# Kernel optimization log

Hardware: AMD Instinct MI355X
Metric: run time of the kernel (lower is better)

## Reference

```python
import jax, jax.numpy as jnp
import numpy as np

N_NODES = 100000
N_EDGES = 1200000
N_GRAPHS = 2048
VOCAB = 10000
D = 64
C = 2


def setup_inputs() -> dict:
    key = jax.random.key(0)
    ks = jax.random.split(key, 12)
    x = jax.random.randint(ks[0], (N_NODES,), 0, VOCAB)
    edge_index = jax.random.randint(ks[1], (2, N_EDGES), 0, N_NODES)
    batch = jnp.sort(jax.random.randint(ks[2], (N_NODES,), 0, N_GRAPHS))
    s = 0.1
    return {
        'x': x,
        'edge_index': edge_index,
        'batch': batch,
        'emb': jax.random.normal(ks[3], (VOCAB, D), jnp.float32) * s,
        'W1l': jax.random.normal(ks[4], (D, D), jnp.float32) * s,
        'b1l': jnp.zeros((D,), jnp.float32),
        'W1r': jax.random.normal(ks[5], (D, D), jnp.float32) * s,
        'W2l': jax.random.normal(ks[6], (D, D), jnp.float32) * s,
        'b2l': jnp.zeros((D,), jnp.float32),
        'W2r': jax.random.normal(ks[7], (D, D), jnp.float32) * s,
        'Wout': jax.random.normal(ks[8], (C, D), jnp.float32) * s,
        'bout': jnp.zeros((C,), jnp.float32),
    }


def _sage(h, src, dst, Wl, bl, Wr, n_nodes):
    # mean aggregation of source messages onto target nodes (PyG SAGEConv, aggr='mean')
    agg = jax.ops.segment_sum(h[src], dst, num_segments=n_nodes)  # [N, D]
    cnt = jax.ops.segment_sum(jnp.ones((src.shape[0],), h.dtype), dst, num_segments=n_nodes)
    agg = agg / jnp.maximum(cnt, 1.0)[:, None]
    # lin_l(agg) + lin_r(root); lin_l carries the bias, lin_r has none
    return agg @ Wl.T + bl + h @ Wr.T


def reference(x, edge_index, batch, emb, W1l, b1l, W1r, W2l, b2l, W2r, Wout, bout):
    src, dst = edge_index[0], edge_index[1]
    h = emb[x]                                   # [N, D] embedding lookup
    h = jax.nn.relu(_sage(h, src, dst, W1l, b1l, W1r, N_NODES))
    h = jax.nn.relu(_sage(h, src, dst, W2l, b2l, W2r, N_NODES))
    # global mean pool per graph
    pooled = jax.ops.segment_sum(h, batch, num_segments=N_GRAPHS)
    gcnt = jax.ops.segment_sum(jnp.ones((N_NODES,), h.dtype), batch, num_segments=N_GRAPHS)
    pooled = pooled / jnp.maximum(gcnt, 1.0)[:, None]
    return pooled @ Wout.T + bout                # [G, C]
```

## Files before the change

### kernel.cpp

```cpp
#include <hip/hip_runtime.h>

#define NN 100000
#define NE 1200000
#define NG 2048
#define VOCAB 10000
#define D 64
#define C 2

#define NBK 196
#define BSH 9
#define SLOT 7168

typedef _Float16 half8 __attribute__((ext_vector_type(8)));
typedef _Float16 half2 __attribute__((ext_vector_type(2)));

#if __has_builtin(__builtin_amdgcn_fdot2)
#define FDOT2(a, b, c) __builtin_amdgcn_fdot2((a), (b), (c), false)
#else
#define FDOT2(a, b, c) ((float)(a)[0] * (float)(b)[0] + (float)(a)[1] * (float)(b)[1] + (c))
#endif

__device__ __forceinline__ int atomAddI(int* p, int v) {
    return __hip_atomic_fetch_add(p, v, __ATOMIC_RELAXED, __HIP_MEMORY_SCOPE_AGENT);
}
__device__ __forceinline__ void atomAddF(float* p, float v) {
    __hip_atomic_fetch_add(p, v, __ATOMIC_RELAXED, __HIP_MEMORY_SCOPE_AGENT);
}

__global__ void __launch_bounds__(256) k_prepb(const float4* __restrict__ emb4,
        half8* __restrict__ embh,
        const float* __restrict__ W1l, const float* __restrict__ W1r,
        const float* __restrict__ W2l, const float* __restrict__ W2r,
        half2* __restrict__ wp,
        const int* __restrict__ batch, int* __restrict__ gs,
        const int* __restrict__ src, const int* __restrict__ dst,
        int* __restrict__ bcur, unsigned* __restrict__ barr) {
    int blk = blockIdx.x;
    int tid = threadIdx.x;
    if (blk < 313) {
        int i = blk * 256 + tid;
        if (i >= VOCAB * 8) return;
        float4 a = emb4[(size_t)i * 2], b = emb4[(size_t)i * 2 + 1];
        half8 h;
        h[0] = (_Float16)a.x; h[1] = (_Float16)a.y; h[2] = (_Float16)a.z; h[3] = (_Float16)a.w;
        h[4] = (_Float16)b.x; h[5] = (_Float16)b.y; h[6] = (_Float16)b.z; h[7] = (_Float16)b.w;
        embh[i] = h;
    } else if (blk < 345) {
        int i = (blk - 313) * 256 + tid;
        if (i >= 4 * 2048) return;
        int mat = i >> 11, idx = i & 2047;
        const float* W = (mat == 0) ? W1l : (mat == 1) ? W1r : (mat == 2) ? W2l : W2r;
        int row = idx >> 5, kk = idx & 31;
        half2 o;
        o[0] = (_Float16)W[row * 64 + 2 * kk];
        o[1] = (_Float16)W[row * 64 + 2 * kk + 1];
        wp[i] = o;
    } else if (blk < 736) {
        int n = (blk - 345) * 256 + tid;
        if (n >= NN) return;
        int b = batch[n];
        if (n == 0) {
            for (int g = 0; g <= b; ++g) gs[g] = 0;
        } else {
            int bp = batch[n - 1];
            for (int g = bp + 1; g <= b; ++g) gs[g] = n;
        }
        if (n == NN - 1) {
            for (int g = b + 1; g <= NG; ++g) gs[g] = NN;
        }
    } else {
        __shared__ int hcnt[NBK], hbase[NBK], hrank[NBK];
        if (tid < NBK) { hcnt[tid] = 0; hrank[tid] = 0; }
        __syncthreads();
        int bb = blk - 736;
        int per = NE / 384;
        int e0 = bb * per, e1 = e0 + per;
        for (int e = e0 + tid; e < e1; e += 256)
            atomicAdd(&hcnt[dst[e] >> BSH], 1);
        __syncthreads();
        if (tid < NBK) {
            int c = hcnt[tid];
            hbase[tid] = c ? atomAddI(&bcur[tid], c) : 0;
        }
        __syncthreads();
        for (int e = e0 + tid; e < e1; e += 256) {
            int d = dst[e], s = src[e];
            int b = d >> BSH;
            int r = atomicAdd(&hrank[b], 1);
            barr[(size_t)b * SLOT + hbase[b] + r] = ((unsigned)s << BSH) | (unsigned)(d & 511);
        }
    }
}

__global__ void __launch_bounds__(512) k_sortb(const int* __restrict__ bcur,
        const unsigned* __restrict__ barr, const int* __restrict__ x,
        int* __restrict__ start, int* __restrict__ csr, unsigned short* __restrict__ xcsr) {
    __shared__ int cnt[512], loc[512], sm[512];
    int t = threadIdx.x;
    int b = blockIdx.x;
    sm[t] = (t < b && t < NBK) ? bcur[t] : 0;
    cnt[t] = 0;
    __syncthreads();
    for (int off = 1; off < 512; off <<= 1) {
        int v = (t >= off) ? sm[t - off] : 0;
        __syncthreads();
        sm[t] += v;
        __syncthreads();
    }
    int base = sm[511];
    int count = bcur[b];
    const unsigned* bp = barr + (size_t)b * SLOT;
    for (int i = t; i < count; i += 512)
        atomicAdd(&cnt[bp[i] & 511], 1);
    __syncthreads();
    int own = cnt[t];
    sm[t] = own;
    __syncthreads();
    for (int off = 1; off < 512; off <<= 1) {
        int v = (t >= off) ? sm[t - off] : 0;
        __syncthreads();
        sm[t] += v;
        __syncthreads();
    }
    int ex = sm[t] - own;
    loc[t] = ex;
    int g0 = b << BSH;
    if (g0 + t < NN) start[g0 + t] = base + ex;
    if (b == NBK - 1 && t == 0) start[NN] = NE;
    __syncthreads();
    for (int i = t; i < count; i += 512) {
        unsigned p = bp[i];
        int r = atomicAdd(&loc[p & 511], 1);
        int sn = (int)(p >> BSH);
        csr[base + r]  = sn;
        xcsr[base + r] = (unsigned short)x[sn];
    }
}

template<typename IDX>
__device__ __forceinline__ half8 gather_sum(const IDX* __restrict__ idx,
        const half8* __restrict__ g, int f, int s0, int s1) {
    half8 acc = {};
    if (s1 <= s0) return acc;
    const half8 z = {};
    int last = s1 - 1;
    for (int i = s0; i < s1; i += 8) {
        int i1 = min(i + 1, last), i2 = min(i + 2, last), i3 = min(i + 3, last);
        int i4 = min(i + 4, last), i5 = min(i + 5, last), i6 = min(i + 6, last);
        int i7 = min(i + 7, last);
        half8 v0 = g[(size_t)idx[i]  * 8 + f];
        half8 v1 = g[(size_t)idx[i1] * 8 + f];
        half8 v2 = g[(size_t)idx[i2] * 8 + f];
        half8 v3 = g[(size_t)idx[i3] * 8 + f];
        half8 v4 = g[(size_t)idx[i4] * 8 + f];
        half8 v5 = g[(size_t)idx[i5] * 8 + f];
        half8 v6 = g[(size_t)idx[i6] * 8 + f];
        half8 v7 = g[(size_t)idx[i7] * 8 + f];
        v1 = (i + 1 < s1) ? v1 : z;
        v2 = (i + 2 < s1) ? v2 : z;
        v3 = (i + 3 < s1) ? v3 : z;
        v4 = (i + 4 < s1) ? v4 : z;
        v5 = (i + 5 < s1) ? v5 : z;
        v6 = (i + 6 < s1) ? v6 : z;
        v7 = (i + 7 < s1) ? v7 : z;
        acc += ((v0 + v1) + (v2 + v3)) + ((v4 + v5) + (v6 + v7));
    }
    return acc;
}

__global__ void __launch_bounds__(256) k_l1(const int* __restrict__ start,
        const unsigned short* __restrict__ idx, const half8* __restrict__ embh,
        const int* __restrict__ x,
        const half2* __restrict__ wl, const float* __restrict__ bl,
        const half2* __restrict__ wr, half8* __restrict__ h1) {
    __shared__ half8 smA[64][8];
    int tid = threadIdx.x;
    int lane = tid & 63, wave = tid >> 6;

    float pf = 0.f;
    {
        int i = blockIdx.x * 256 + tid;
        if (i < VOCAB * 8) { float4 v = ((const float4*)embh)[i]; pf = v.x * 0.f; }
    }
    asm volatile("" : "+v"(pf));

    int f = lane & 7;
#pragma unroll
    for (int r = 0; r < 2; ++r) {
        int nl = r * 32 + wave * 8 + (lane >> 3);
        int n = blockIdx.x * 64 + nl;
        if (n < NN) {
            int s0 = start[n], s1 = start[n + 1];
            float inv = 1.0f / (float)max(s1 - s0, 1) + pf;
            half8 acc = gather_sum(idx, embh, f, s0, s1);
            half8 o;
#pragma unroll
            for (int k = 0; k < 8; ++k) o[k] = (_Float16)((float)acc[k] * inv);
            smA[nl][f ^ (nl & 7)] = o;
        }
    }
    __syncthreads();

    int h = __builtin_amdgcn_readfirstlane(wave);
    int nn = blockIdx.x * 64 + lane;
    bool valid = nn < NN;
    int n = valid ? nn : NN - 1;

    float acc[16];
#pragma unroll
    for (int d = 0; d < 16; ++d) acc[d] = bl[h * 16 + d];
    const half8* rp = embh + (size_t)x[n] * 8;
    const half2* wlH = wl + (size_t)h * 16 * 32;
    const half2* wrH = wr + (size_t)h * 16 * 32;

    half8 ah = smA[lane][0 ^ (lane & 7)];
    half8 rh = rp[0];
    for (int c = 0; c < 8; ++c) {
        half2 a2[4] = { __builtin_shufflevector(ah, ah, 0, 1),
                        __builtin_shufflevector(ah, ah, 2, 3),
                        __builtin_shufflevector(ah, ah, 4, 5),
                        __builtin_shufflevector(ah, ah, 6, 7) };
        half2 r2[4] = { __builtin_shufflevector(rh, rh, 0, 1),
                        __builtin_shufflevector(rh, rh, 2, 3),
                        __builtin_shufflevector(rh, rh, 4, 5),
                        __builtin_shufflevector(rh, rh, 6, 7) };
        if (c < 7) {
            ah = smA[lane][(c + 1) ^ (lane & 7)];
            rh = rp[c + 1];
        }
        const half2* wlc = wlH + c * 4;
        const half2* wrc = wrH + c * 4;
#pragma unroll
        for (int d = 0; d < 16; ++d) {
#pragma unroll
            for (int kk = 0; kk < 4; ++kk) {
                acc[d] = FDOT2(a2[kk], wlc[d * 32 + kk], acc[d]);
                acc[d] = FDOT2(r2[kk], wrc[d * 32 + kk], acc[d]);
            }
        }
    }

    if (valid) {
        half8 o0, o1;
#pragma unroll
        for (int k = 0; k < 8; ++k) {
            o0[k] = (_Float16)fmaxf(acc[k], 0.f);
            o1[k] = (_Float16)fmaxf(acc[8 + k], 0.f);
        }
        h1[(size_t)n * 8 + 2 * h]     = o0;
        h1[(size_t)n * 8 + 2 * h + 1] = o1;
    }
}

__global__ void __launch_bounds__(256) k_l2(const int* __restrict__ start,
        const int* __restrict__ idx, const half8* __restrict__ h1,
        const int* __restrict__ batch,
        const half2* __restrict__ wl, const float* __restrict__ bl,
        const half2* __restrict__ wr, float* __restrict__ pooled) {
    __shared__ half8 smA[64][8];
    int tid = threadIdx.x;
    int lane = tid & 63, wave = tid >> 6;

    int f = lane & 7;
#pragma unroll
    for (int r = 0; r < 2; ++r) {
        int nl = r * 32 + wave * 8 + (lane >> 3);
        int n = blockIdx.x * 64 + nl;
        if (n < NN) {
            int s0 = start[n], s1 = start[n + 1];
            float inv = 1.0f / (float)max(s1 - s0, 1);
            half8 acc = gather_sum(idx, h1, f, s0, s1);
            half8 o;
#pragma unroll
            for (int k = 0; k < 8; ++k) o[k] = (_Float16)((float)acc[k] * inv);
            smA[nl][f ^ (nl & 7)] = o;
        }
    }
    __syncthreads();

    int h = __builtin_amdgcn_readfirstlane(wave);
    int nn = blockIdx.x * 64 + lane;
    bool valid = nn < NN;
    int n = valid ? nn : NN - 1;

    float acc[16];
#pragma unroll
    for (int d = 0; d < 16; ++d) acc[d] = bl[h * 16 + d];
    const half8* rp = h1 + (size_t)n * 8;
    const half2* wlH = wl + (size_t)h * 16 * 32;
    const half2* wrH = wr + (size_t)h * 16 * 32;

    half8 ah = smA[lane][0 ^ (lane & 7)];
    half8 rh = rp[0];
    for (int c = 0; c < 8; ++c) {
        half2 a2[4] = { __builtin_shufflevector(ah, ah, 0, 1),
                        __builtin_shufflevector(ah, ah, 2, 3),
                        __builtin_shufflevector(ah, ah, 4, 5),
                        __builtin_shufflevector(ah, ah, 6, 7) };
        half2 r2[4] = { __builtin_shufflevector(rh, rh, 0, 1),
                        __builtin_shufflevector(rh, rh, 2, 3),
                        __builtin_shufflevector(rh, rh, 4, 5),
                        __builtin_shufflevector(rh, rh, 6, 7) };
        if (c < 7) {
            ah = smA[lane][(c + 1) ^ (lane & 7)];
            rh = rp[c + 1];
        }
        const half2* wlc = wlH + c * 4;
        const half2* wrc = wrH + c * 4;
#pragma unroll
        for (int d = 0; d < 16; ++d) {
#pragma unroll
            for (int kk = 0; kk < 4; ++kk) {
                acc[d] = FDOT2(a2[kk], wlc[d * 32 + kk], acc[d]);
                acc[d] = FDOT2(r2[kk], wrc[d * 32 + kk], acc[d]);
            }
        }
    }

    int g = batch[n];
    int g1  = __shfl_up(g, 1);
    int g2  = __shfl_up(g, 2);
    int g4  = __shfl_up(g, 4);
    int g8  = __shfl_up(g, 8);
    int g16 = __shfl_up(g, 16);
    int g32 = __shfl_up(g, 32);
    bool s1  = (lane >= 1)  && (g1 == g);
    bool s2  = (lane >= 2)  && (g2 == g);
    bool s4  = (lane >= 4)  && (g4 == g);
    bool s8  = (lane >= 8)  && (g8 == g);
    bool s16 = (lane >= 16) && (g16 == g);
    bool s32 = (lane >= 32) && (g32 == g);
    int gn = __shfl_down(g, 1);
    bool isLast = (lane == 63) || (gn != g);
    float* pg = pooled + (size_t)g * D + h * 16;
#pragma unroll
    for (int d = 0; d < 16; ++d) {
        float v = valid ? fmaxf(acc[d], 0.f) : 0.f;
        float t;
        t = __shfl_up(v, 1);  v += s1  ? t : 0.f;
        t = __shfl_up(v, 2);  v += s2  ? t : 0.f;
        t = __shfl_up(v, 4);  v += s4  ? t : 0.f;
        t = __shfl_up(v, 8);  v += s8  ? t : 0.f;
        t = __shfl_up(v, 16); v += s16 ? t : 0.f;
        t = __shfl_up(v, 32); v += s32 ? t : 0.f;
        if (isLast) atomAddF(pg + d, v);
    }
}

__global__ void __launch_bounds__(256) k_out(const int* __restrict__ gs,
        const float* __restrict__ pooled, const float* __restrict__ Wout,
        const float* __restrict__ bout, float* __restrict__ out) {
    int lane = threadIdx.x & 63;
    int wave = threadIdx.x >> 6;
    int g = blockIdx.x * 4 + wave;
    int s0 = gs[g], s1 = gs[g + 1];
    float p = pooled[(size_t)g * D + lane] / (float)max(s1 - s0, 1);
    float c0 = p * Wout[lane];
    float c1 = p * Wout[D + lane];
#pragma unroll
    for (int off = 32; off > 0; off >>= 1) {
        c0 += __shfl_down(c0, off, 64);
        c1 += __shfl_down(c1, off, 64);
    }
    if (lane == 0) {
        out[g * C + 0] = c0 + bout[0];
        out[g * C + 1] = c1 + bout[1];
    }
}

extern "C" void kernel_launch(void* const* d_in, const int* in_sizes, int n_in,
                              void* d_out, int out_size, void* d_ws, size_t ws_size,
                              hipStream_t stream) {
    const int*   x     = (const int*)d_in[0];
    const int*   src   = (const int*)d_in[1];
    const int*   dst   = src + NE;
    const int*   batch = (const int*)d_in[2];
    const float* emb   = (const float*)d_in[3];
    const float* W1l   = (const float*)d_in[4];
    const float* b1l   = (const float*)d_in[5];
    const float* W1r   = (const float*)d_in[6];
    const float* W2l   = (const float*)d_in[7];
    const float* b2l   = (const float*)d_in[8];
    const float* W2r   = (const float*)d_in[9];
    const float* Wout  = (const float*)d_in[10];
    const float* bout  = (const float*)d_in[11];
    float* out = (float*)d_out;

    _Float16* T0h  = (_Float16*)d_ws;
    _Float16* embh = T0h + (size_t)NN * 64;
    _Float16* wpck = embh + (size_t)VOCAB * 64;
    float* pooled  = (float*)(wpck + 16384);
    int* bcur   = (int*)(pooled + (size_t)NG * 64);
    int* startA = bcur + NBK;
    int* gs     = startA + NN + 1;
    int* csr    = gs + NG + 1;
    unsigned short* xcsr = (unsigned short*)(csr + NE);
    unsigned* barr = (unsigned*)(xcsr + NE);
    half2* wp = (half2*)wpck;

    hipMemsetAsync(pooled, 0, ((size_t)NG * 64 + NBK) * sizeof(float), stream);

    k_prepb<<<1120, 256, 0, stream>>>((const float4*)emb, (half8*)embh,
                                      W1l, W1r, W2l, W2r, wp, batch, gs,
                                      src, dst, bcur, barr);
    k_sortb<<<NBK, 512, 0, stream>>>(bcur, barr, x, startA, csr, xcsr);

    int fusedGrid = (NN + 63) / 64;
    k_l1<<<fusedGrid, 256, 0, stream>>>(startA, xcsr, (const half8*)embh, x,
                                        wp, b1l, wp + 2048, (half8*)T0h);
    k_l2<<<fusedGrid, 256, 0, stream>>>(startA, csr, (const half8*)T0h, batch,
                                        wp + 4096, b2l, wp + 6144, pooled);

    k_out<<<NG / 4, 256, 0, stream>>>(gs, pooled, Wout, bout, out);
}
```

Before: 202.4 us.

## Replace bucketed two-pass CSR sort with per-node count, scan, and atomic placement

CSR construction no longer bins edges into per-bucket staging slots and then locally sorts each bucket in shared memory. It now counts per-node in-degree with global atomics, derives start offsets with a per-bucket scan, and places each edge with a global atomic cursor in a new kernel. This removes the intermediate staging array and the shared-memory sort pass, at the cost of 1.2M global atomics twice, one extra launch, and a nondeterministic edge order within each node's neighbour list.

```diff
diff --git a/kernel.cpp b/kernel.cpp
--- a/kernel.cpp
+++ b/kernel.cpp
@@ -9,7 +9,6 @@
 
 #define NBK 196
 #define BSH 9
-#define SLOT 7168
 
 typedef _Float16 half8 __attribute__((ext_vector_type(8)));
 typedef _Float16 half2 __attribute__((ext_vector_type(2)));
@@ -33,8 +32,8 @@
         const float* __restrict__ W2l, const float* __restrict__ W2r,
         half2* __restrict__ wp,
         const int* __restrict__ batch, int* __restrict__ gs,
-        const int* __restrict__ src, const int* __restrict__ dst,
-        int* __restrict__ bcur, unsigned* __restrict__ barr) {
+        const int* __restrict__ dst,
+        int* __restrict__ bcur, int* __restrict__ ncnt) {
     int blk = blockIdx.x;
     int tid = threadIdx.x;
     if (blk < 313) {
@@ -69,37 +68,31 @@
             for (int g = b + 1; g <= NG; ++g) gs[g] = NN;
         }
     } else {
-        __shared__ int hcnt[NBK], hbase[NBK], hrank[NBK];
-        if (tid < NBK) { hcnt[tid] = 0; hrank[tid] = 0; }
+        __shared__ int hcnt[NBK];
+        if (tid < NBK) hcnt[tid] = 0;
         __syncthreads();
         int bb = blk - 736;
         int per = NE / 384;
         int e0 = bb * per, e1 = e0 + per;
-        for (int e = e0 + tid; e < e1; e += 256)
-            atomicAdd(&hcnt[dst[e] >> BSH], 1);
+        for (int e = e0 + tid; e < e1; e += 256) {
+            int d = dst[e];
+            atomicAdd(&hcnt[d >> BSH], 1);
+            atomAddI(&ncnt[d], 1);
+        }
         __syncthreads();
         if (tid < NBK) {
             int c = hcnt[tid];
-            hbase[tid] = c ? atomAddI(&bcur[tid], c) : 0;
-        }
-        __syncthreads();
-        for (int e = e0 + tid; e < e1; e += 256) {
-            int d = dst[e], s = src[e];
-            int b = d >> BSH;
-            int r = atomicAdd(&hrank[b], 1);
-            barr[(size_t)b * SLOT + hbase[b] + r] = ((unsigned)s << BSH) | (unsigned)(d & 511);
-        }
-    }
-}
-
-__global__ void __launch_bounds__(512) k_sortb(const int* __restrict__ bcur,
-        const unsigned* __restrict__ barr, const int* __restrict__ x,
-        int* __restrict__ start, int* __restrict__ csr, unsigned short* __restrict__ xcsr) {
-    __shared__ int cnt[512], loc[512], sm[512];
+            if (c) atomAddI(&bcur[tid], c);
+        }
+    }
+}
+
+__global__ void __launch_bounds__(512) k_scan(const int* __restrict__ bcur,
+        const int* __restrict__ ncnt, int* __restrict__ start, int* __restrict__ cur) {
+    __shared__ int sm[512];
     int t = threadIdx.x;
     int b = blockIdx.x;
     sm[t] = (t < b && t < NBK) ? bcur[t] : 0;
-    cnt[t] = 0;
     __syncthreads();
     for (int off = 1; off < 512; off <<= 1) {
         int v = (t >= off) ? sm[t - off] : 0;
@@ -108,13 +101,11 @@
         __syncthreads();
     }
     int base = sm[511];
-    int count = bcur[b];
-    const unsigned* bp = barr + (size_t)b * SLOT;
-    for (int i = t; i < count; i += 512)
-        atomicAdd(&cnt[bp[i] & 511], 1);
     __syncthreads();
-    int own = cnt[t];
-    sm[t] = own;
+    int g0 = b << BSH;
+    int n = g0 + t;
+    int deg = (n < NN) ? ncnt[n] : 0;
+    sm[t] = deg;
     __syncthreads();
     for (int off = 1; off < 512; off <<= 1) {
         int v = (t >= off) ? sm[t - off] : 0;
@@ -122,18 +113,24 @@
         sm[t] += v;
         __syncthreads();
     }
-    int ex = sm[t] - own;
-    loc[t] = ex;
-    int g0 = b << BSH;
-    if (g0 + t < NN) start[g0 + t] = base + ex;
+    int ex = sm[t] - deg;
+    if (n < NN) {
+        start[n] = base + ex;
+        cur[n]   = base + ex;
+    }
     if (b == NBK - 1 && t == 0) start[NN] = NE;
-    __syncthreads();
-    for (int i = t; i < count; i += 512) {
-        unsigned p = bp[i];
-        int r = atomicAdd(&loc[p & 511], 1);
-        int sn = (int)(p >> BSH);
-        csr[base + r]  = sn;
-        xcsr[base + r] = (unsigned short)x[sn];
+}
+
+__global__ void __launch_bounds__(256) k_place(const int* __restrict__ src,
+        const int* __restrict__ dst, const int* __restrict__ x,
+        int* __restrict__ cur, int* __restrict__ csr, unsigned short* __restrict__ xcsr) {
+    int e = blockIdx.x * 256 + threadIdx.x;
+    int stride = gridDim.x * 256;
+    for (; e < NE; e += stride) {
+        int d = dst[e], s = src[e];
+        int pos = atomAddI(&cur[d], 1);
+        csr[pos]  = s;
+        xcsr[pos] = (unsigned short)x[s];
     }
 }
 
@@ -391,19 +388,21 @@
     _Float16* wpck = embh + (size_t)VOCAB * 64;
     float* pooled  = (float*)(wpck + 16384);
     int* bcur   = (int*)(pooled + (size_t)NG * 64);
-    int* startA = bcur + NBK;
-    int* gs     = startA + NN + 1;
+    int* ncnt   = bcur + NBK;
+    int* startA = ncnt + NN;
+    int* cur    = startA + NN + 1;
+    int* gs     = cur + NN;
     int* csr    = gs + NG + 1;
     unsigned short* xcsr = (unsigned short*)(csr + NE);
-    unsigned* barr = (unsigned*)(xcsr + NE);
     half2* wp = (half2*)wpck;
 
-    hipMemsetAsync(pooled, 0, ((size_t)NG * 64 + NBK) * sizeof(float), stream);
+    hipMemsetAsync(pooled, 0, ((size_t)NG * 64 + NBK + NN) * sizeof(float), stream);
 
     k_prepb<<<1120, 256, 0, stream>>>((const float4*)emb, (half8*)embh,
                                       W1l, W1r, W2l, W2r, wp, batch, gs,
-                                      src, dst, bcur, barr);
-    k_sortb<<<NBK, 512, 0, stream>>>(bcur, barr, x, startA, csr, xcsr);
+                                      dst, bcur, ncnt);
+    k_scan <<<NBK, 512, 0, stream>>>(bcur, ncnt, startA, cur);
+    k_place<<<1172, 256, 0, stream>>>(src, dst, x, cur, csr, xcsr);
 
     int fusedGrid = (NN + 63) / 64;
     k_l1<<<fusedGrid, 256, 0, stream>>>(startA, xcsr, (const half8*)embh, x,
```

Result: slower. 292.4 us (+44.4%).
